# Kernel tuning notes

Measured on AMD Instinct MI355X. Metric: run time of the kernel, lower is better.

## Reference

```python
import jax, jax.numpy as jnp
import numpy as np

T, BATCH, DIM = 2048, 32, 512

def setup_inputs() -> dict:
    key = jax.random.key(0)
    ks = jax.random.split(key, 9)
    s = 1.0 / np.sqrt(DIM)
    return {
        "x": jax.random.normal(ks[0], (T, BATCH, DIM), dtype=jnp.float32),
        "W_in": jax.random.uniform(ks[1], (2 * DIM, DIM), jnp.float32, -s, s),
        "b_in": jax.random.uniform(ks[2], (2 * DIM,), jnp.float32, -s, s),
        "W_out": jax.random.uniform(ks[3], (DIM, DIM), jnp.float32, -s, s),
        "b_out": jax.random.uniform(ks[4], (DIM,), jnp.float32, -s, s),
        "A": jax.random.normal(ks[5], (DIM,), dtype=jnp.float32) * 0.1,
        "B": jax.random.normal(ks[6], (DIM,), dtype=jnp.float32) * 0.1,
        "gamma": jnp.ones((DIM,), dtype=jnp.float32),
        "beta": jnp.zeros((DIM,), dtype=jnp.float32),
    }

def _layernorm(y, gamma, beta, eps=1e-5):
    mu = jnp.mean(y, axis=-1, keepdims=True)
    var = jnp.mean(jnp.square(y - mu), axis=-1, keepdims=True)
    return (y - mu) * jax.lax.rsqrt(var + eps) * gamma + beta

def reference(x, W_in, b_in, W_out, b_out, A, B, gamma, beta):
    # in_proj then chunk along last dim: z first half, g second half
    zg = jnp.einsum('tbd,ed->tbe', x, W_in) + b_in          # [T,B,2D]
    z, g = jnp.split(zg, 2, axis=-1)
    g = jax.nn.sigmoid(g)
    Bz = B * z                                              # [T,B,D]
    gA = g * A                                              # [T,B,D]

    # diagonal linear recurrence h_t = gA_t * h_{t-1} + Bz_t
    def step(prev, inp):
        ga_t, bz_t = inp
        curr = ga_t * prev + bz_t
        return curr, curr

    h0 = jnp.zeros((x.shape[1], x.shape[2]), dtype=x.dtype)
    _, h = jax.lax.scan(step, h0, (gA, Bz))                 # [T,B,D]

    out = jnp.einsum('tbd,ed->tbe', h, W_out) + b_out
    return _layernorm(x + out, gamma, beta)
```

## Files before the change

### kernel.cpp

```cpp
#include <hip/hip_runtime.h>
#include <hip/hip_bf16.h>
#include <cstdint>
#include <cstddef>

#define T_LEN 2048
#define BATCH 32
#define DIM 512
#define M_TOT (T_LEN * BATCH)
#define K_DIM DIM
#define N1 (2 * DIM)
#define NCHUNK 64
#define CLEN (T_LEN / NCHUNK)
#define BD (BATCH * DIM)
#define MT_TILES (M_TOT / 128)

typedef unsigned short ushort_t;
typedef __attribute__((ext_vector_type(8))) short short8;
typedef __attribute__((ext_vector_type(4))) float floatx4;
typedef __attribute__((ext_vector_type(4))) unsigned short ushort4v;

__device__ __forceinline__ float bf2f(ushort_t u) {
  union { unsigned int i; float f; } v;
  v.i = ((unsigned int)u) << 16;
  return v.f;
}
__device__ __forceinline__ ushort_t f2bf(float f) {
  union { float f; unsigned int i; } v;
  v.f = f;
  unsigned int x = v.i;
  return (ushort_t)((x + 0x7fffu + ((x >> 16) & 1u)) >> 16);
}

__device__ __forceinline__ void async16(const void* gp, void* lp) {
  __builtin_amdgcn_global_load_lds(
      (__attribute__((address_space(1))) void*)(void*)gp,
      (__attribute__((address_space(3))) void*)lp, 16, 0, 0);
}

__global__ __launch_bounds__(256) void cvt_f32_bf16(const float* __restrict__ in,
                                                    ushort_t* __restrict__ out,
                                                    int n4) {
  int i = blockIdx.x * 256 + threadIdx.x;
  if (i >= n4) return;
  const floatx4 v = *((const floatx4*)in + i);
  ushort4v o;
  o.x = f2bf(v.x); o.y = f2bf(v.y); o.z = f2bf(v.z); o.w = f2bf(v.w);
  *((ushort4v*)out + i) = o;
}

template <int MODE, int NT>
__global__ __launch_bounds__(256, 2) void gemm_bt(
    const ushort_t* __restrict__ Ag, const ushort_t* __restrict__ Bg,
    const float* __restrict__ bias, const float* __restrict__ Avec,
    const float* __restrict__ Bvec, ushort_t* __restrict__ out0,
    ushort_t* __restrict__ out1) {
  __shared__ __align__(16) ushort_t As[128 * 64];
  __shared__ __align__(16) ushort_t Bs[128 * 64];
  const int tid = threadIdx.x;
  const int lane = tid & 63;
  const int wid = tid >> 6;
  const int wave_m = wid >> 1;
  const int wave_n = wid & 1;

  const int bid = blockIdx.x;
  const int xcd = bid & 7;
  const int slot = bid >> 3;
  const int mt = xcd * (MT_TILES / 8) + slot / NT;
  const int nt = slot % NT;
  const int m0 = mt * 128;
  const int n0 = nt * 128;

  floatx4 acc[4][4] = {};

  const int sr = tid >> 3;
  const int sc = tid & 7;

  for (int k0 = 0; k0 < K_DIM; k0 += 64) {
    __syncthreads();
#pragma unroll
    for (int i = 0; i < 4; i++) {
      const int r = i * 32 + sr;
      const int cg = sc ^ (r & 7);
      async16(Ag + (size_t)(m0 + r) * K_DIM + k0 + cg * 8,
              (char*)As + (i * 32 + wid * 8) * 128);
      async16(Bg + (size_t)(n0 + r) * K_DIM + k0 + cg * 8,
              (char*)Bs + (i * 32 + wid * 8) * 128);
    }
    __syncthreads();
#pragma unroll
    for (int kk = 0; kk < 2; kk++) {
      const int jc = kk * 4 + (lane >> 4);
      short8 af[4], bfr[4];
#pragma unroll
      for (int im = 0; im < 4; im++) {
        const int row = wave_m * 64 + im * 16 + (lane & 15);
        af[im] = *(const short8*)((const char*)As + row * 128 +
                                  ((jc ^ (row & 7)) * 16));
      }
#pragma unroll
      for (int in = 0; in < 4; in++) {
        const int row = wave_n * 64 + in * 16 + (lane & 15);
        bfr[in] = *(const short8*)((const char*)Bs + row * 128 +
                                   ((jc ^ (row & 7)) * 16));
      }
#pragma unroll
      for (int im = 0; im < 4; im++)
#pragma unroll
        for (int in = 0; in < 4; in++)
          acc[im][in] = __builtin_amdgcn_mfma_f32_16x16x32_bf16(
              af[im], bfr[in], acc[im][in], 0, 0, 0);
    }
  }

#pragma unroll
  for (int im = 0; im < 4; im++) {
#pragma unroll
    for (int in = 0; in < 4; in++) {
      const int col = n0 + wave_n * 64 + in * 16 + (lane & 15);
#pragma unroll
      for (int r = 0; r < 4; r++) {
        const int row = m0 + wave_m * 64 + im * 16 + (lane >> 4) * 4 + r;
        float val = acc[im][in][r] + bias[col];
        if (MODE == 0) {
          if (col < DIM) {
            out0[(size_t)row * DIM + col] = f2bf(Bvec[col] * val);
          } else {
            const int d = col - DIM;
            const float s = 1.f / (1.f + __expf(-val));
            out1[(size_t)row * DIM + d] = f2bf(Avec[d] * s);
          }
        } else {
          out0[(size_t)row * DIM + col] = f2bf(val);
        }
      }
    }
  }
}


__global__ __launch_bounds__(256) void scan_pass1(
    const ushort_t* __restrict__ a_arr, const ushort_t* __restrict__ bz_arr,
    float* __restrict__ pout, float* __restrict__ hout) {
  const int tid = blockIdx.x * 256 + threadIdx.x;
  const int c = tid >> 12;
  const int q = tid & 4095;
  size_t base = (size_t)(c * CLEN) * BD + q * 4;
  float h0 = 0.f, h1 = 0.f, h2 = 0.f, h3 = 0.f;
  float p0 = 1.f, p1 = 1.f, p2 = 1.f, p3 = 1.f;
#pragma unroll 8
  for (int t = 0; t < CLEN; t++) {
    ushort4v av = *(const ushort4v*)(a_arr + base + (size_t)t * BD);
    ushort4v bv = *(const ushort4v*)(bz_arr + base + (size_t)t * BD);
    float a0 = bf2f(av.x), a1 = bf2f(av.y), a2 = bf2f(av.z), a3 = bf2f(av.w);
    h0 = a0 * h0 + bf2f(bv.x); p0 *= a0;
    h1 = a1 * h1 + bf2f(bv.y); p1 *= a1;
    h2 = a2 * h2 + bf2f(bv.z); p2 *= a2;
    h3 = a3 * h3 + bf2f(bv.w); p3 *= a3;
  }
  const size_t ci = (size_t)c * BD + q * 4;
  *(floatx4*)(pout + ci) = (floatx4){p0, p1, p2, p3};
  *(floatx4*)(hout + ci) = (floatx4){h0, h1, h2, h3};
}

__global__ __launch_bounds__(256) void scan_pass2(
    const float* __restrict__ p, const float* __restrict__ hend,
    float* __restrict__ carry) {
  const int q = blockIdx.x * 256 + threadIdx.x;
  float h0 = 0.f, h1 = 0.f, h2 = 0.f, h3 = 0.f;
  for (int c = 0; c < NCHUNK; c++) {
    const size_t ci = (size_t)c * BD + q * 4;
    floatx4 pv = *(const floatx4*)(p + ci);
    floatx4 hv = *(const floatx4*)(hend + ci);
    *(floatx4*)(carry + ci) = (floatx4){h0, h1, h2, h3};
    h0 = hv.x + pv.x * h0;
    h1 = hv.y + pv.y * h1;
    h2 = hv.z + pv.z * h2;
    h3 = hv.w + pv.w * h3;
  }
}

__global__ __launch_bounds__(256) void scan_pass3(
    const ushort_t* __restrict__ a_arr, const ushort_t* __restrict__ bz_arr,
    const float* __restrict__ carry, ushort_t* __restrict__ h_arr) {
  const int tid = blockIdx.x * 256 + threadIdx.x;
  const int c = tid >> 12;
  const int q = tid & 4095;
  size_t base = (size_t)(c * CLEN) * BD + q * 4;
  const size_t ci = (size_t)c * BD + q * 4;
  floatx4 cv = *(const floatx4*)(carry + ci);
  float h0 = cv.x, h1 = cv.y, h2 = cv.z, h3 = cv.w;
#pragma unroll 8
  for (int t = 0; t < CLEN; t++) {
    ushort4v av = *(const ushort4v*)(a_arr + base + (size_t)t * BD);
    ushort4v bv = *(const ushort4v*)(bz_arr + base + (size_t)t * BD);
    h0 = bf2f(av.x) * h0 + bf2f(bv.x);
    h1 = bf2f(av.y) * h1 + bf2f(bv.y);
    h2 = bf2f(av.z) * h2 + bf2f(bv.z);
    h3 = bf2f(av.w) * h3 + bf2f(bv.w);
    ushort4v o;
    o.x = f2bf(h0); o.y = f2bf(h1); o.z = f2bf(h2); o.w = f2bf(h3);
    *(ushort4v*)(h_arr + base + (size_t)t * BD) = o;
  }
}

__global__ __launch_bounds__(256) void ln_kernel(
    const float* __restrict__ x, const ushort_t* __restrict__ op,
    const float* __restrict__ gamma, const float* __restrict__ beta,
    float* __restrict__ y) {
  const int wid = threadIdx.x >> 6;
  const int lane = threadIdx.x & 63;
  const size_t row = (size_t)blockIdx.x * 4 + wid;
  const size_t base = row * DIM + lane * 8;
  floatx4 x0 = *(const floatx4*)(x + base);
  floatx4 x1 = *(const floatx4*)(x + base + 4);
  short8 ov = *(const short8*)(op + base);
  float v[8];
  v[0] = x0.x + bf2f((ushort_t)ov[0]);
  v[1] = x0.y + bf2f((ushort_t)ov[1]);
  v[2] = x0.z + bf2f((ushort_t)ov[2]);
  v[3] = x0.w + bf2f((ushort_t)ov[3]);
  v[4] = x1.x + bf2f((ushort_t)ov[4]);
  v[5] = x1.y + bf2f((ushort_t)ov[5]);
  v[6] = x1.z + bf2f((ushort_t)ov[6]);
  v[7] = x1.w + bf2f((ushort_t)ov[7]);
  float s = 0.f, ss = 0.f;
#pragma unroll
  for (int j = 0; j < 8; j++) {
    s += v[j];
    ss += v[j] * v[j];
  }
#pragma unroll
  for (int m = 32; m >= 1; m >>= 1) {
    s += __shfl_xor(s, m, 64);
    ss += __shfl_xor(ss, m, 64);
  }
  const float mean = s * (1.f / DIM);
  const float var = ss * (1.f / DIM) - mean * mean;
  const float rstd = rsqrtf(var + 1e-5f);
  const int cb = lane * 8;
  floatx4 o0, o1;
  o0.x = (v[0] - mean) * rstd * gamma[cb + 0] + beta[cb + 0];
  o0.y = (v[1] - mean) * rstd * gamma[cb + 1] + beta[cb + 1];
  o0.z = (v[2] - mean) * rstd * gamma[cb + 2] + beta[cb + 2];
  o0.w = (v[3] - mean) * rstd * gamma[cb + 3] + beta[cb + 3];
  o1.x = (v[4] - mean) * rstd * gamma[cb + 4] + beta[cb + 4];
  o1.y = (v[5] - mean) * rstd * gamma[cb + 5] + beta[cb + 5];
  o1.z = (v[6] - mean) * rstd * gamma[cb + 6] + beta[cb + 6];
  o1.w = (v[7] - mean) * rstd * gamma[cb + 7] + beta[cb + 7];
  *(floatx4*)(y + base) = o0;
  *(floatx4*)(y + base + 4) = o1;
}

extern "C" void kernel_launch(void* const* d_in, const int* in_sizes, int n_in,
                              void* d_out, int out_size, void* d_ws,
                              size_t ws_size, hipStream_t stream) {
  const float* x = (const float*)d_in[0];
  const float* W_in = (const float*)d_in[1];
  const float* b_in = (const float*)d_in[2];
  const float* W_out = (const float*)d_in[3];
  const float* b_out = (const float*)d_in[4];
  const float* Avec = (const float*)d_in[5];
  const float* Bvec = (const float*)d_in[6];
  const float* gamma = (const float*)d_in[7];
  const float* beta = (const float*)d_in[8];
  float* out = (float*)d_out;

  char* ws = (char*)d_ws;
  const size_t SZ64 = (size_t)M_TOT * DIM * 2;
  ushort_t* xb = (ushort_t*)ws;
  ushort_t* gA = (ushort_t*)(ws + SZ64);
  ushort_t* bz = (ushort_t*)(ws + 2 * SZ64);
  ushort_t* wib = (ushort_t*)(ws + 3 * SZ64);
  ushort_t* wob = (ushort_t*)(ws + 3 * SZ64 + (size_t)N1 * K_DIM * 2);
  char* p0 = ws + 3 * SZ64 + (size_t)N1 * K_DIM * 2 + (size_t)DIM * K_DIM * 2;
  float* pc = (float*)p0;
  float* hc = (float*)(p0 + (size_t)NCHUNK * BD * 4);
  float* cc = (float*)(p0 + 2 * (size_t)NCHUNK * BD * 4);

  cvt_f32_bf16<<<(M_TOT * DIM / 4 + 255) / 256, 256, 0, stream>>>(
      x, xb, M_TOT * DIM / 4);
  cvt_f32_bf16<<<(N1 * K_DIM / 4 + 255) / 256, 256, 0, stream>>>(
      W_in, wib, N1 * K_DIM / 4);
  cvt_f32_bf16<<<(DIM * K_DIM / 4 + 255) / 256, 256, 0, stream>>>(
      W_out, wob, DIM * K_DIM / 4);

  gemm_bt<0, 8><<<MT_TILES * 8, 256, 0, stream>>>(
      xb, wib, b_in, Avec, Bvec, bz, gA);

  scan_pass1<<<NCHUNK * (BD / 4) / 256, 256, 0, stream>>>(gA, bz, pc, hc);
  scan_pass2<<<(BD / 4) / 256, 256, 0, stream>>>(pc, hc, cc);
  scan_pass3<<<NCHUNK * (BD / 4) / 256, 256, 0, stream>>>(gA, bz, cc, xb);

  gemm_bt<1, 4><<<MT_TILES * 4, 256, 0, stream>>>(
      xb, wob, b_out, nullptr, nullptr, gA, nullptr);

  ln_kernel<<<M_TOT / 4, 256, 0, stream>>>(x, gA, gamma, beta, out);
}
```

Before: 495.0 us.

## Enlarge GEMM tiles to 256x256 with double-buffered LDS async prefetch

```diff
diff --git a/kernel.cpp b/kernel.cpp
--- a/kernel.cpp
+++ b/kernel.cpp
@@ -12,7 +12,7 @@
 #define NCHUNK 64
 #define CLEN (T_LEN / NCHUNK)
 #define BD (BATCH * DIM)
-#define MT_TILES (M_TOT / 128)
+#define MT256 (M_TOT / 256)
 
 typedef unsigned short ushort_t;
 typedef __attribute__((ext_vector_type(8))) short short8;
@@ -36,6 +36,8 @@
       (__attribute__((address_space(1))) void*)(void*)gp,
       (__attribute__((address_space(3))) void*)lp, 16, 0, 0);
 }
+
+#define WAITVM(N) asm volatile("s_waitcnt vmcnt(" #N ")" ::: "memory")
 
 __global__ __launch_bounds__(256) void cvt_f32_bf16(const float* __restrict__ in,
                                                     ushort_t* __restrict__ out,
@@ -49,77 +51,94 @@
 }
 
 template <int MODE, int NT>
-__global__ __launch_bounds__(256, 2) void gemm_bt(
+__global__ __launch_bounds__(512, 2) void gemm_bt(
     const ushort_t* __restrict__ Ag, const ushort_t* __restrict__ Bg,
     const float* __restrict__ bias, const float* __restrict__ Avec,
     const float* __restrict__ Bvec, ushort_t* __restrict__ out0,
     ushort_t* __restrict__ out1) {
-  __shared__ __align__(16) ushort_t As[128 * 64];
-  __shared__ __align__(16) ushort_t Bs[128 * 64];
+  __shared__ __align__(16) ushort_t As[2][256 * 64];
+  __shared__ __align__(16) ushort_t Bs[2][256 * 64];
   const int tid = threadIdx.x;
   const int lane = tid & 63;
   const int wid = tid >> 6;
-  const int wave_m = wid >> 1;
-  const int wave_n = wid & 1;
+  const int wave_m = wid >> 2;
+  const int wave_n = wid & 3;
 
   const int bid = blockIdx.x;
   const int xcd = bid & 7;
   const int slot = bid >> 3;
-  const int mt = xcd * (MT_TILES / 8) + slot / NT;
+  const int mt = xcd * (MT256 / 8) + slot / NT;
   const int nt = slot % NT;
-  const int m0 = mt * 128;
-  const int n0 = nt * 128;
-
-  floatx4 acc[4][4] = {};
+  const int m0 = mt * 256;
+  const int n0 = nt * 256;
+
+  floatx4 acc[8][4] = {};
 
   const int sr = tid >> 3;
   const int sc = tid & 7;
 
-  for (int k0 = 0; k0 < K_DIM; k0 += 64) {
-    __syncthreads();
+  auto stage = [&](int kt, int s) {
+    const int k0 = kt * 64;
 #pragma unroll
     for (int i = 0; i < 4; i++) {
-      const int r = i * 32 + sr;
+      const int r = i * 64 + sr;
       const int cg = sc ^ (r & 7);
       async16(Ag + (size_t)(m0 + r) * K_DIM + k0 + cg * 8,
-              (char*)As + (i * 32 + wid * 8) * 128);
+              (char*)(&As[s][0]) + (i * 64 + wid * 8) * 128);
       async16(Bg + (size_t)(n0 + r) * K_DIM + k0 + cg * 8,
-              (char*)Bs + (i * 32 + wid * 8) * 128);
+              (char*)(&Bs[s][0]) + (i * 64 + wid * 8) * 128);
     }
-    __syncthreads();
+  };
+
+  stage(0, 0);
+
+  for (int t = 0; t < K_DIM / 64; ++t) {
+    if (t < K_DIM / 64 - 1) {
+      stage(t + 1, (t + 1) & 1);
+      WAITVM(8);
+    } else {
+      WAITVM(0);
+    }
+    __builtin_amdgcn_s_barrier();
+    __builtin_amdgcn_sched_barrier(0);
+
+    const ushort_t* Asl = &As[t & 1][0];
+    const ushort_t* Bsl = &Bs[t & 1][0];
 #pragma unroll
     for (int kk = 0; kk < 2; kk++) {
       const int jc = kk * 4 + (lane >> 4);
-      short8 af[4], bfr[4];
-#pragma unroll
-      for (int im = 0; im < 4; im++) {
-        const int row = wave_m * 64 + im * 16 + (lane & 15);
-        af[im] = *(const short8*)((const char*)As + row * 128 +
+      short8 af[8], bfr[4];
+#pragma unroll
+      for (int im = 0; im < 8; im++) {
+        const int row = wave_m * 128 + im * 16 + (lane & 15);
+        af[im] = *(const short8*)((const char*)Asl + row * 128 +
                                   ((jc ^ (row & 7)) * 16));
       }
 #pragma unroll
       for (int in = 0; in < 4; in++) {
         const int row = wave_n * 64 + in * 16 + (lane & 15);
-        bfr[in] = *(const short8*)((const char*)Bs + row * 128 +
+        bfr[in] = *(const short8*)((const char*)Bsl + row * 128 +
                                    ((jc ^ (row & 7)) * 16));
       }
 #pragma unroll
-      for (int im = 0; im < 4; im++)
+      for (int im = 0; im < 8; im++)
 #pragma unroll
         for (int in = 0; in < 4; in++)
           acc[im][in] = __builtin_amdgcn_mfma_f32_16x16x32_bf16(
               af[im], bfr[in], acc[im][in], 0, 0, 0);
     }
-  }
-
-#pragma unroll
-  for (int im = 0; im < 4; im++) {
+    __builtin_amdgcn_sched_barrier(0);
+    __builtin_amdgcn_s_barrier();
+  }
+
+#pragma unroll
+  for (int im = 0; im < 8; im++) {
 #pragma unroll
     for (int in = 0; in < 4; in++) {
       const int col = n0 + wave_n * 64 + in * 16 + (lane & 15);
 #pragma unroll
       for (int r = 0; r < 4; r++) {
-        const int row = m0 + wave_m * 64 + im * 16 + (lane >> 4) * 4 + r;
+        const int row = m0 + wave_m * 128 + im * 16 + (lane >> 4) * 4 + r;
         float val = acc[im][in][r] + bias[col];
         if (MODE == 0) {
           if (col < DIM) {
@@ -284,14 +303,14 @@
   cvt_f32_bf16<<<(DIM * K_DIM / 4 + 255) / 256, 256, 0, stream>>>(
       W_out, wob, DIM * K_DIM / 4);
 
-  gemm_bt<0, 8><<<MT_TILES * 8, 256, 0, stream>>>(
+  gemm_bt<0, 4><<<MT256 * 4, 512, 0, stream>>>(
       xb, wib, b_in, Avec, Bvec, bz, gA);
 
   scan_pass1<<<NCHUNK * (BD / 4) / 256, 256, 0, stream>>>(gA, bz, pc, hc);
   scan_pass2<<<(BD / 4) / 256, 256, 0, stream>>>(pc, hc, cc);
   scan_pass3<<<NCHUNK * (BD / 4) / 256, 256, 0, stream>>>(gA, bz, cc, xb);
 
-  gemm_bt<1, 4><<<MT_TILES * 4, 256, 0, stream>>>(
+  gemm_bt<1, 2><<<MT256 * 2, 512, 0, stream>>>(
       xb, wob, b_out, nullptr, nullptr, gA, nullptr);
 
   ln_kernel<<<M_TOT / 4, 256, 0, stream>>>(x, gA, gamma, beta, out);
```

Result: slower. 543.1 us (+9.7%).

## Fuse output GEMM with residual LayerNorm and widen scan vectorization

Applied to the files above, without the earlier changes.

```diff
diff --git a/kernel.cpp b/kernel.cpp
--- a/kernel.cpp
+++ b/kernel.cpp
@@ -48,8 +48,7 @@
   *((ushort4v*)out + i) = o;
 }
 
-template <int MODE, int NT>
-__global__ __launch_bounds__(256, 2) void gemm_bt(
+__global__ __launch_bounds__(256, 2) void gemm_in(
     const ushort_t* __restrict__ Ag, const ushort_t* __restrict__ Bg,
     const float* __restrict__ bias, const float* __restrict__ Avec,
     const float* __restrict__ Bvec, ushort_t* __restrict__ out0,
@@ -65,8 +64,8 @@
   const int bid = blockIdx.x;
   const int xcd = bid & 7;
   const int slot = bid >> 3;
-  const int mt = xcd * (MT_TILES / 8) + slot / NT;
-  const int nt = slot % NT;
+  const int mt = xcd * (MT_TILES / 8) + slot / 8;
+  const int nt = slot % 8;
   const int m0 = mt * 128;
   const int n0 = nt * 128;
 
@@ -121,17 +120,130 @@
       for (int r = 0; r < 4; r++) {
         const int row = m0 + wave_m * 64 + im * 16 + (lane >> 4) * 4 + r;
         float val = acc[im][in][r] + bias[col];
-        if (MODE == 0) {
-          if (col < DIM) {
-            out0[(size_t)row * DIM + col] = f2bf(Bvec[col] * val);
-          } else {
-            const int d = col - DIM;
-            const float s = 1.f / (1.f + __expf(-val));
-            out1[(size_t)row * DIM + d] = f2bf(Avec[d] * s);
-          }
+        if (col < DIM) {
+          out0[(size_t)row * DIM + col] = f2bf(Bvec[col] * val);
         } else {
-          out0[(size_t)row * DIM + col] = f2bf(val);
+          const int d = col - DIM;
+          const float s = 1.f / (1.f + __expf(-val));
+          out1[(size_t)row * DIM + d] = f2bf(Avec[d] * s);
         }
+      }
+    }
+  }
+}
+
+__global__ __launch_bounds__(512, 4) void gemm_ln(
+    const ushort_t* __restrict__ Ag,
+    const ushort_t* __restrict__ Bg,
+    const float* __restrict__ bias,
+    const float* __restrict__ x,
+    const float* __restrict__ gamma, const float* __restrict__ beta,
+    float* __restrict__ out) {
+  __shared__ __align__(16) ushort_t As[64 * 64];
+  __shared__ __align__(16) ushort_t Bs[512 * 64];
+  __shared__ float red[64][8][2];
+  __shared__ float stat[64][2];
+  const int tid = threadIdx.x;
+  const int lane = tid & 63;
+  const int wid = tid >> 6;
+  const int m0 = blockIdx.x * 64;
+
+  floatx4 acc[4][4] = {};
+  const int sr = tid >> 3;
+  const int sc = tid & 7;
+
+  for (int k0 = 0; k0 < K_DIM; k0 += 64) {
+    __syncthreads();
+    {
+      const int cg = sc ^ (sr & 7);
+      async16(Ag + (size_t)(m0 + sr) * K_DIM + k0 + cg * 8,
+              (char*)As + tid * 16);
+    }
+#pragma unroll
+    for (int i = 0; i < 8; i++) {
+      const int r = i * 64 + sr;
+      const int cg = sc ^ (r & 7);
+      async16(Bg + (size_t)r * K_DIM + k0 + cg * 8,
+              (char*)Bs + i * 8192 + tid * 16);
+    }
+    __syncthreads();
+#pragma unroll
+    for (int kk = 0; kk < 2; kk++) {
+      const int jc = kk * 4 + (lane >> 4);
+      short8 af[4], bfr[4];
+#pragma unroll
+      for (int im = 0; im < 4; im++) {
+        const int row = im * 16 + (lane & 15);
+        af[im] = *(const short8*)((const char*)As + row * 128 +
+                                  ((jc ^ (row & 7)) * 16));
+      }
+#pragma unroll
+      for (int in = 0; in < 4; in++) {
+        const int row = wid * 64 + in * 16 + (lane & 15);
+        bfr[in] = *(const short8*)((const char*)Bs + row * 128 +
+                                   ((jc ^ (row & 7)) * 16));
+      }
+#pragma unroll
+      for (int im = 0; im < 4; im++)
+#pragma unroll
+        for (int in = 0; in < 4; in++)
+          acc[im][in] = __builtin_amdgcn_mfma_f32_16x16x32_bf16(
+              af[im], bfr[in], acc[im][in], 0, 0, 0);
+    }
+  }
+
+  float bcol[4];
+#pragma unroll
+  for (int in = 0; in < 4; in++)
+    bcol[in] = bias[wid * 64 + in * 16 + (lane & 15)];
+
+#pragma unroll
+  for (int im = 0; im < 4; im++) {
+#pragma unroll
+    for (int r = 0; r < 4; r++) {
+      const int rowl = im * 16 + (lane >> 4) * 4 + r;
+      const size_t rowg = (size_t)(m0 + rowl);
+      float s = 0.f, ss = 0.f;
+#pragma unroll
+      for (int in = 0; in < 4; in++) {
+        const int col = wid * 64 + in * 16 + (lane & 15);
+        const float y = x[rowg * DIM + col] + acc[im][in][r] + bcol[in];
+        s += y; ss += y * y;
+      }
+#pragma unroll
+      for (int m = 8; m >= 1; m >>= 1) {
+        s += __shfl_xor(s, m, 64);
+        ss += __shfl_xor(ss, m, 64);
+      }
+      if ((lane & 15) == 0) {
+        red[rowl][wid][0] = s;
+        red[rowl][wid][1] = ss;
+      }
+    }
+  }
+  __syncthreads();
+  if (tid < 64) {
+    float s = 0.f, ss = 0.f;
+#pragma unroll
+    for (int w = 0; w < 8; w++) { s += red[tid][w][0]; ss += red[tid][w][1]; }
+    const float mean = s * (1.f / DIM);
+    const float var = ss * (1.f / DIM) - mean * mean;
+    stat[tid][0] = mean;
+    stat[tid][1] = rsqrtf(var + 1e-5f);
+  }
+  __syncthreads();
+#pragma unroll
+  for (int im = 0; im < 4; im++) {
+#pragma unroll
+    for (int r = 0; r < 4; r++) {
+      const int rowl = im * 16 + (lane >> 4) * 4 + r;
+      const size_t rowg = (size_t)(m0 + rowl);
+      const float mean = stat[rowl][0], rstd = stat[rowl][1];
+#pragma unroll
+      for (int in = 0; in < 4; in++) {
+        const int col = wid * 64 + in * 16 + (lane & 15);
+        const float y = x[rowg * DIM + col] + acc[im][in][r] + bcol[in];
+        out[rowg * DIM + col] = (y - mean) * rstd * gamma[col] + beta[col];
       }
     }
   }
@@ -142,40 +254,42 @@
     const ushort_t* __restrict__ a_arr, const ushort_t* __restrict__ bz_arr,
     float* __restrict__ pout, float* __restrict__ hout) {
   const int tid = blockIdx.x * 256 + threadIdx.x;
-  const int c = tid >> 12;
-  const int q = tid & 4095;
-  size_t base = (size_t)(c * CLEN) * BD + q * 4;
-  float h0 = 0.f, h1 = 0.f, h2 = 0.f, h3 = 0.f;
-  float p0 = 1.f, p1 = 1.f, p2 = 1.f, p3 = 1.f;
-#pragma unroll 8
+  const int c = tid >> 11;
+  const int q = tid & 2047;
+  size_t base = (size_t)(c * CLEN) * BD + q * 8;
+  float h[8], p[8];
+#pragma unroll
+  for (int j = 0; j < 8; j++) { h[j] = 0.f; p[j] = 1.f; }
+#pragma unroll 4
   for (int t = 0; t < CLEN; t++) {
-    ushort4v av = *(const ushort4v*)(a_arr + base + (size_t)t * BD);
-    ushort4v bv = *(const ushort4v*)(bz_arr + base + (size_t)t * BD);
-    float a0 = bf2f(av.x), a1 = bf2f(av.y), a2 = bf2f(av.z), a3 = bf2f(av.w);
-    h0 = a0 * h0 + bf2f(bv.x); p0 *= a0;
-    h1 = a1 * h1 + bf2f(bv.y); p1 *= a1;
-    h2 = a2 * h2 + bf2f(bv.z); p2 *= a2;
-    h3 = a3 * h3 + bf2f(bv.w); p3 *= a3;
-  }
-  const size_t ci = (size_t)c * BD + q * 4;
-  *(floatx4*)(pout + ci) = (floatx4){p0, p1, p2, p3};
-  *(floatx4*)(hout + ci) = (floatx4){h0, h1, h2, h3};
+    short8 av = *(const short8*)(a_arr + base + (size_t)t * BD);
+    short8 bv = *(const short8*)(bz_arr + base + (size_t)t * BD);
+#pragma unroll
+    for (int j = 0; j < 8; j++) {
+      const float a = bf2f((ushort_t)av[j]);
+      h[j] = a * h[j] + bf2f((ushort_t)bv[j]);
+      p[j] *= a;
+    }
+  }
+  const size_t ci = (size_t)c * BD + q * 8;
+  *(floatx4*)(pout + ci) = (floatx4){p[0], p[1], p[2], p[3]};
+  *(floatx4*)(pout + ci + 4) = (floatx4){p[4], p[5], p[6], p[7]};
+  *(floatx4*)(hout + ci) = (floatx4){h[0], h[1], h[2], h[3]};
+  *(floatx4*)(hout + ci + 4) = (floatx4){h[4], h[5], h[6], h[7]};
 }
 
 __global__ __launch_bounds__(256) void scan_pass2(
     const float* __restrict__ p, const float* __restrict__ hend,
     float* __restrict__ carry) {
   const int q = blockIdx.x * 256 + threadIdx.x;
-  float h0 = 0.f, h1 = 0.f, h2 = 0.f, h3 = 0.f;
+  float h = 0.f;
+#pragma unroll 4
   for (int c = 0; c < NCHUNK; c++) {
-    const size_t ci = (size_t)c * BD + q * 4;
-    floatx4 pv = *(const floatx4*)(p + ci);
-    floatx4 hv = *(const floatx4*)(hend + ci);
-    *(floatx4*)(carry + ci) = (floatx4){h0, h1, h2, h3};
-    h0 = hv.x + pv.x * h0;
-    h1 = hv.y + pv.y * h1;
-    h2 = hv.z + pv.z * h2;
-    h3 = hv.w + pv.w * h3;
+    const size_t ci = (size_t)c * BD + q;
+    const float pv = p[ci];
+    const float hv = hend[ci];
+    carry[ci] = h;
+    h = hv + pv * h;
   }
 }
 
@@ -183,72 +297,25 @@
     const ushort_t* __restrict__ a_arr, const ushort_t* __restrict__ bz_arr,
     const float* __restrict__ carry, ushort_t* __restrict__ h_arr) {
   const int tid = blockIdx.x * 256 + threadIdx.x;
-  const int c = tid >> 12;
-  const int q = tid & 4095;
-  size_t base = (size_t)(c * CLEN) * BD + q * 4;
-  const size_t ci = (size_t)c * BD + q * 4;
-  floatx4 cv = *(const floatx4*)(carry + ci);
-  float h0 = cv.x, h1 = cv.y, h2 = cv.z, h3 = cv.w;
-#pragma unroll 8
+  const int c = tid >> 11;
+  const int q = tid & 2047;
+  size_t base = (size_t)(c * CLEN) * BD + q * 8;
+  const size_t ci = (size_t)c * BD + q * 8;
+  floatx4 c0 = *(const floatx4*)(carry + ci);
+  floatx4 c1 = *(const floatx4*)(carry + ci + 4);
+  float h[8] = {c0.x, c0.y, c0.z, c0.w, c1.x, c1.y, c1.z, c1.w};
+#pragma unroll 4
   for (int t = 0; t < CLEN; t++) {
-    ushort4v av = *(const ushort4v*)(a_arr + base + (size_t)t * BD);
-    ushort4v bv = *(const ushort4v*)(bz_arr + base + (size_t)t * BD);
-    h0 = bf2f(av.x) * h0 + bf2f(bv.x);
-    h1 = bf2f(av.y) * h1 + bf2f(bv.y);
-    h2 = bf2f(av.z) * h2 + bf2f(bv.z);
-    h3 = bf2f(av.w) * h3 + bf2f(bv.w);
-    ushort4v o;
-    o.x = f2bf(h0); o.y = f2bf(h1); o.z = f2bf(h2); o.w = f2bf(h3);
-    *(ushort4v*)(h_arr + base + (size_t)t * BD) = o;
-  }
-}
-
-__global__ __launch_bounds__(256) void ln_kernel(
-    const float* __restrict__ x, const ushort_t* __restrict__ op,
-    const float* __restrict__ gamma, const float* __restrict__ beta,
-    float* __restrict__ y) {
-  const int wid = threadIdx.x >> 6;
-  const int lane = threadIdx.x & 63;
-  const size_t row = (size_t)blockIdx.x * 4 + wid;
-  const size_t base = row * DIM + lane * 8;
-  floatx4 x0 = *(const floatx4*)(x + base);
-  floatx4 x1 = *(const floatx4*)(x + base + 4);
-  short8 ov = *(const short8*)(op + base);
-  float v[8];
-  v[0] = x0.x + bf2f((ushort_t)ov[0]);
-  v[1] = x0.y + bf2f((ushort_t)ov[1]);
-  v[2] = x0.z + bf2f((ushort_t)ov[2]);
-  v[3] = x0.w + bf2f((ushort_t)ov[3]);
-  v[4] = x1.x + bf2f((ushort_t)ov[4]);
-  v[5] = x1.y + bf2f((ushort_t)ov[5]);
-  v[6] = x1.z + bf2f((ushort_t)ov[6]);
-  v[7] = x1.w + bf2f((ushort_t)ov[7]);
-  float s = 0.f, ss = 0.f;
-#pragma unroll
-  for (int j = 0; j < 8; j++) {
-    s += v[j];
-    ss += v[j] * v[j];
-  }
-#pragma unroll
-  for (int m = 32; m >= 1; m >>= 1) {
-    s += __shfl_xor(s, m, 64);
-    ss += __shfl_xor(ss, m, 64);
-  }
-  const float mean = s * (1.f / DIM);
-  const float var = ss * (1.f / DIM) - mean * mean;
-  const float rstd = rsqrtf(var + 1e-5f);
-  const int cb = lane * 8;
-  floatx4 o0, o1;
-  o0.x = (v[0] - mean) * rstd * gamma[cb + 0] + beta[cb + 0];
-  o0.y = (v[1] - mean) * rstd * gamma[cb + 1] + beta[cb + 1];
-  o0.z = (v[2] - mean) * rstd * gamma[cb + 2] + beta[cb + 2];
-  o0.w = (v[3] - mean) * rstd * gamma[cb + 3] + beta[cb + 3];
-  o1.x = (v[4] - mean) * rstd * gamma[cb + 4] + beta[cb + 4];
-  o1.y = (v[5] - mean) * rstd * gamma[cb + 5] + beta[cb + 5];
-  o1.z = (v[6] - mean) * rstd * gamma[cb + 6] + beta[cb + 6];
-  o1.w = (v[7] - mean) * rstd * gamma[cb + 7] + beta[cb + 7];
-  *(floatx4*)(y + base) = o0;
-  *(floatx4*)(y + base + 4) = o1;
+    short8 av = *(const short8*)(a_arr + base + (size_t)t * BD);
+    short8 bv = *(const short8*)(bz_arr + base + (size_t)t * BD);
+    short8 o;
+#pragma unroll
+    for (int j = 0; j < 8; j++) {
+      h[j] = bf2f((ushort_t)av[j]) * h[j] + bf2f((ushort_t)bv[j]);
+      o[j] = (short)f2bf(h[j]);
+    }
+    *(short8*)(h_arr + base + (size_t)t * BD) = o;
+  }
 }
 
 extern "C" void kernel_launch(void* const* d_in, const int* in_sizes, int n_in,
@@ -284,15 +351,13 @@
   cvt_f32_bf16<<<(DIM * K_DIM / 4 + 255) / 256, 256, 0, stream>>>(
       W_out, wob, DIM * K_DIM / 4);
 
-  gemm_bt<0, 8><<<MT_TILES * 8, 256, 0, stream>>>(
+  gemm_in<<<MT_TILES * 8, 256, 0, stream>>>(
       xb, wib, b_in, Avec, Bvec, bz, gA);
 
-  scan_pass1<<<NCHUNK * (BD / 4) / 256, 256, 0, stream>>>(gA, bz, pc, hc);
-  scan_pass2<<<(BD / 4) / 256, 256, 0, stream>>>(pc, hc, cc);
-  scan_pass3<<<NCHUNK * (BD / 4) / 256, 256, 0, stream>>>(gA, bz, cc, xb);
-
-  gemm_bt<1, 4><<<MT_TILES * 4, 256, 0, stream>>>(
-      xb, wob, b_out, nullptr, nullptr, gA, nullptr);
-
-  ln_kernel<<<M_TOT / 4, 256, 0, stream>>>(x, gA, gamma, beta, out);
-}
+  scan_pass1<<<NCHUNK * (BD / 8) / 256, 256, 0, stream>>>(gA, bz, pc, hc);
+  scan_pass2<<<BD / 256, 256, 0, stream>>>(pc, hc, cc);
+  scan_pass3<<<NCHUNK * (BD / 8) / 256, 256, 0, stream>>>(gA, bz, cc, xb);
+
+  gemm_ln<<<M_TOT / 64, 512, 0, stream>>>(
+      xb, wob, b_out, x, gamma, beta, out);
+}
```

Measured after the change: 558.4 us. 1.13x slower.
